# Kernel tuning notes

Measured on AMD Instinct MI355X. Metric: run time of the kernel, lower is better.

Reference implementation:

```python
import jax, jax.numpy as jnp
import numpy as np

TEMPERATURE = 0.03


def setup_inputs() -> dict:
    key = jax.random.key(0)
    k1, k2, k3 = jax.random.split(key, 3)
    B, d = 8192, 256
    z_a = jax.random.normal(k1, (B, d), dtype=jnp.float32)
    z_t = jax.random.normal(k2, (B, d), dtype=jnp.float32)
    # module expects L2-normalized projections
    z_a = z_a / jnp.linalg.norm(z_a, axis=-1, keepdims=True)
    z_t = z_t / jnp.linalg.norm(z_t, axis=-1, keepdims=True)
    patient_ids = jax.random.randint(k3, (B,), 0, 2048, dtype=jnp.int64)
    return {"z_a": z_a, "z_t": z_t, "patient_ids": patient_ids}


def _direction_loss(sim, cross_mask):
    # sim: (B, B) row i = anchor i vs all candidates; cross_mask: (B, B) valid negatives
    B = sim.shape[0]
    pos = jnp.diagonal(sim)                              # (B,) positive logits
    logit_mask = cross_mask | jnp.eye(B, dtype=bool)     # negatives + the positive
    lse = jax.nn.logsumexp(sim, axis=1, where=logit_mask)  # (B,)
    row_loss = lse - pos                                 # CE with label = positive
    valid = cross_mask.any(axis=1)                       # rows with >=1 cross-patient neg
    cnt = jnp.sum(valid)
    total = jnp.sum(jnp.where(valid, row_loss, 0.0))
    return jnp.where(cnt > 0, total / jnp.maximum(cnt, 1).astype(sim.dtype), 0.0)


def reference(z_a, z_t, patient_ids):
    sim = jnp.matmul(z_a, z_t.T) / TEMPERATURE           # (B, B)
    cross = patient_ids[:, None] != patient_ids[None, :] # cross-patient negative mask
    loss_a2t = _direction_loss(sim, cross)
    loss_t2a = _direction_loss(sim.T, cross.T)
    return (loss_a2t + loss_t2a) / 2.0
```

## Files before the change

### kernel.cpp

```cpp
#include <hip/hip_runtime.h>
#include <math.h>

#define BSZ    8192
#define DDIM   256
#define SCALE  33.33333333333333f
#define C_OFF  34.0f
#define SC_L2E 48.08983470f
#define C2     49.05163139f

typedef float floatx4  __attribute__((ext_vector_type(4)));
typedef float floatx16 __attribute__((ext_vector_type(16)));
typedef int   intx4    __attribute__((ext_vector_type(4)));
typedef int   intx8    __attribute__((ext_vector_type(8)));
typedef long long fp8x8;

__device__ __forceinline__ fp8x8 cvt8_f8(const float* __restrict__ g)
{
    const float4 lo = *(const float4*)g;
    const float4 hi = *(const float4*)(g + 4);
    int a = __builtin_amdgcn_cvt_pk_fp8_f32(lo.x, lo.y, 0, false);
    a     = __builtin_amdgcn_cvt_pk_fp8_f32(lo.z, lo.w, a, true);
    int b = __builtin_amdgcn_cvt_pk_fp8_f32(hi.x, hi.y, 0, false);
    b     = __builtin_amdgcn_cvt_pk_fp8_f32(hi.z, hi.w, b, true);
    int2 r; r.x = a; r.y = b;
    return *(fp8x8*)&r;
}

__global__ __launch_bounds__(256) void prep_kernel(
    const float* __restrict__ za, const float* __restrict__ zt,
    unsigned char* __restrict__ za_f8, unsigned char* __restrict__ zt_perm,
    float* __restrict__ zbase)
{
    const int bid = blockIdx.x, tid = threadIdx.x;
    if (bid < 1024) {
        const int i = (bid * 256 + tid) * 8;
        *(fp8x8*)(za_f8 + i) = cvt8_f8(za + i);
        if (bid < 16) {
            const int z = bid * 1024 + tid * 4;
            *(float4*)&zbase[z] = (float4){0.f, 0.f, 0.f, 0.f};
            if (bid == 0 && tid == 0) {
                zbase[16384] = 0.f;
                ((int*)zbase)[16385] = 0;
                ((int*)zbase)[16386] = 0;
            }
        }
    } else {
        const int S    = (bid - 1024) * 256 + tid;
        const int cbb  = S >> 12;
        const int col  = (S >> 5) & 127;
        const int gph  = (S >> 1) & 15;
        const int off8 = (S & 1) * 8;
        const int k    = ((gph ^ (col & 15)) << 4) + off8;
        const float* src = zt + (size_t)(cbb * 128 + col) * DDIM + k;
        *(fp8x8*)(zt_perm + (size_t)S * 8) = cvt8_f8(src);
    }
}

__global__ __launch_bounds__(256, 2) void sim_fused(
    const unsigned char* __restrict__ za_f8, const unsigned char* __restrict__ zt_perm,
    const int* __restrict__ pid,
    float* __restrict__ s_row, float* __restrict__ s_col,
    float* __restrict__ posv)
{
    __shared__ __align__(16) unsigned char Bs[32768];
    __shared__ int   pidc[128];
    __shared__ float colsum[128];

    const int bid   = blockIdx.x;
    const int cbb   = bid & 63;
    const int bgrp  = bid >> 6;
    const int col0g = cbb * 128;
    const int tid   = threadIdx.x, lane = tid & 63, wid = tid >> 6;
    const int l31   = lane & 31, h = lane >> 5;

    if (tid < 128) { pidc[tid] = pid[col0g + tid]; colsum[tid] = 0.f; }

    {
        const unsigned char* src = zt_perm + (size_t)cbb * 32768 + wid * 8192 + lane * 16;
        unsigned char* dst = Bs + wid * 8192 + lane * 16;
        #pragma unroll
        for (int i = 0; i < 8; i++)
            __builtin_amdgcn_global_load_lds(
                (const __attribute__((address_space(1))) void*)(src + i * 1024),
                (__attribute__((address_space(3))) void*)(dst + i * 1024),
                16, 0, 0);
    }

    const int band0 = bgrp * 8;
    intx8 afc[4];
    {
        const unsigned char* ga =
            za_f8 + (size_t)(band0 * 128 + wid * 32 + l31) * DDIM + h * 32;
        #pragma unroll
        for (int ks = 0; ks < 4; ks++)
            afc[ks] = *(const intx8*)(ga + ks * 64);
    }

    __syncthreads();

    const int t16 = ((((lane >> 4) & 2) ^ (lane & 15)) << 4);
    int dsb[4];
    #pragma unroll
    for (int n = 0; n < 4; n++)
        dsb[n] = n * 8192 + l31 * 256 + t16;

    int pc[4];
    #pragma unroll
    for (int n = 0; n < 4; n++) pc[n] = pidc[n * 32 + l31];

    float colp4[4] = {0.f, 0.f, 0.f, 0.f};
    const int  target = (lane & 3) + 4 * ((lane >> 3) & 3);
    const bool ownl   = (h == ((lane >> 2) & 1));

    #pragma unroll
    for (int i = 0; i < 8; i++) {
        const int band  = band0 + i;
        const int rbase = band * 128 + wid * 32;

        intx8 afn[4];
        if (i < 7) {
            const unsigned char* ga =
                za_f8 + (size_t)(rbase + 128 + l31) * DDIM + h * 32;
            #pragma unroll
            for (int ks = 0; ks < 4; ks++)
                afn[ks] = *(const intx8*)(ga + ks * 64);
        }

        int prw[16];
        #pragma unroll
        for (int reg = 0; reg < 16; reg++)
            prw[reg] = pid[rbase + (reg & 3) + 8 * (reg >> 2) + 4 * h];

        floatx16 acc[4];
        #pragma unroll
        for (int n = 0; n < 4; n++) acc[n] = (floatx16)0.0f;

        #pragma unroll
        for (int ks = 0; ks < 4; ks++) {
            #pragma unroll
            for (int n = 0; n < 4; n++) {
                intx4 lo = *(const intx4*)(Bs + (dsb[n] ^ ((ks * 4 + 0) << 4)));
                intx4 hi = *(const intx4*)(Bs + (dsb[n] ^ ((ks * 4 + 1) << 4)));
                intx8 b;
                b[0] = lo[0]; b[1] = lo[1]; b[2] = lo[2]; b[3] = lo[3];
                b[4] = hi[0]; b[5] = hi[1]; b[6] = hi[2]; b[7] = hi[3];
                acc[n] = __builtin_amdgcn_mfma_scale_f32_32x32x64_f8f6f4(
                    afc[ks], b, acc[n], 0, 0, 0, 0x7F7F7F7F, 0, 0x7F7F7F7F);
            }
        }

        float rowp[16];
        #pragma unroll
        for (int r = 0; r < 16; r++) rowp[r] = 0.f;

        #pragma unroll
        for (int n = 0; n < 4; n++) {
            const int pcn = pc[n];
            #pragma unroll
            for (int reg = 0; reg < 16; reg++) {
                float e = __builtin_amdgcn_exp2f(fmaf(acc[n][reg], SC_L2E, -C2));
                e = (prw[reg] != pcn) ? e : 0.f;
                colp4[n] += e;
                rowp[reg] += e;
            }
            if (band == cbb && n == wid) {
                float vd = 0.f;
                #pragma unroll
                for (int reg = 0; reg < 16; reg++)
                    vd = (reg == target) ? acc[n][reg] : vd;
                float ed = __builtin_amdgcn_exp2f(fmaf(vd, SC_L2E, -C2));
                ed = ownl ? ed : 0.f;
                colp4[n] += ed;
                #pragma unroll
                for (int reg = 0; reg < 16; reg++)
                    rowp[reg] += (reg == target) ? ed : 0.f;
                if (ownl) posv[band * 128 + wid * 32 + l31] = vd * SCALE;
            }
        }

#define RED(bit, c)                                                        \
        _Pragma("unroll")                                                  \
        for (int _i = 0; _i < (c); _i++) {                                 \
            float _s = (lane & (bit)) ? rowp[_i] : rowp[_i + (c)];         \
            float _o = __shfl_xor(_s, (bit), 64);                          \
            rowp[_i] = ((lane & (bit)) ? rowp[_i + (c)] : rowp[_i]) + _o;  \
        }
        RED(1, 8) RED(2, 4) RED(4, 2) RED(8, 1)
#undef RED
        rowp[0] += __shfl_xor(rowp[0], 16, 64);
        if ((lane & 16) == 0) {
            const int reg = ((lane & 1) << 3) | ((lane & 2) << 1)
                          | ((lane & 4) >> 1) | ((lane & 8) >> 3);
            const int rl  = (reg & 3) + 8 * (reg >> 2) + 4 * h;
            atomicAdd(&s_row[rbase + rl], rowp[0]);
        }

        if (i < 7) {
            #pragma unroll
            for (int ks = 0; ks < 4; ks++) afc[ks] = afn[ks];
        }
    }

    #pragma unroll
    for (int n = 0; n < 4; n++)
        colp4[n] += __shfl_xor(colp4[n], 32, 64);
    if (lane < 32) {
        #pragma unroll
        for (int n = 0; n < 4; n++)
            atomicAdd(&colsum[n * 32 + lane], colp4[n]);
    }
    __syncthreads();
    if (tid < 128) atomicAdd(&s_col[col0g + tid], colsum[tid]);
}

__global__ __launch_bounds__(256) void finalize_rows(
    const int* __restrict__ pid,
    const float* __restrict__ s_row, const float* __restrict__ s_col,
    const float* __restrict__ posv,
    float* __restrict__ total, int* __restrict__ flag, int* __restrict__ cnt,
    float* __restrict__ out)
{
    const int i = blockIdx.x * 256 + threadIdx.x;
    const float p = posv[i];
    const float c = (logf(s_row[i]) + C_OFF - p)
                  + (logf(s_col[i]) + C_OFF - p);

    float v = c;
    #pragma unroll
    for (int off = 32; off > 0; off >>= 1) v += __shfl_down(v, off, 64);
    if ((threadIdx.x & 63) == 0) atomicAdd(total, v);

    const unsigned long long m = __ballot(pid[i] != pid[0]);
    if (m != 0ull && (threadIdx.x & 63) == 0) atomicOr(flag, 1);

    __syncthreads();
    __threadfence();
    if (threadIdx.x == 0) {
        const int done = atomicAdd(cnt, 1);
        if (done == (int)gridDim.x - 1) {
            const float t = atomicAdd(total, 0.0f);
            const int   f = atomicOr(flag, 0);
            out[0] = f ? t / (2.0f * (float)BSZ) : 0.0f;
        }
    }
}

extern "C" void kernel_launch(void* const* d_in, const int* in_sizes, int n_in,
                              void* d_out, int out_size, void* d_ws, size_t ws_size,
                              hipStream_t stream)
{
    const float* za  = (const float*)d_in[0];
    const float* zt  = (const float*)d_in[1];
    const int*   pid = (const int*)d_in[2];
    float* out = (float*)d_out;

    unsigned char* za_f8   = (unsigned char*)d_ws;
    unsigned char* zt_perm = za_f8 + (size_t)BSZ * DDIM;
    float*  s_row   = (float*)(zt_perm + (size_t)BSZ * DDIM);
    float*  s_col   = s_row + BSZ;
    float*  total   = s_col + BSZ;
    int*    flag    = (int*)(total + 1);
    int*    cnt     = flag + 1;
    float*  posv    = (float*)(cnt + 1);

    prep_kernel<<<dim3(2048), 256, 0, stream>>>(za, zt, za_f8, zt_perm, s_row);

    sim_fused<<<dim3(512), 256, 0, stream>>>(za_f8, zt_perm, pid,
                                             s_row, s_col, posv);

    finalize_rows<<<dim3(BSZ / 256), 256, 0, stream>>>(
        pid, s_row, s_col, posv, total, flag, cnt, out);
}
```

Measured before the change: 102.0 us.

## Fold finalize into sim kernel via grid-wide atomic counter barrier

Removes the separate finalize_rows launch. Each sim_fused block bumps a global counter when it finishes, and the first 32 blocks spin until all 512 blocks are done, then read the row and column sums and the positives atomically and reduce the loss. B-fragment loading is also rewritten as two direct vector stores. This trades a kernel launch for a spin-wait that relies on all 512 blocks being co-resident (2 per CU) to avoid deadlock.

```diff
diff --git a/kernel.cpp b/kernel.cpp
--- a/kernel.cpp
+++ b/kernel.cpp
@@ -42,6 +42,7 @@
                 zbase[16384] = 0.f;
                 ((int*)zbase)[16385] = 0;
                 ((int*)zbase)[16386] = 0;
+                ((int*)zbase)[16387] = 0;
             }
         }
     } else {
@@ -60,7 +61,10 @@
     const unsigned char* __restrict__ za_f8, const unsigned char* __restrict__ zt_perm,
     const int* __restrict__ pid,
     float* __restrict__ s_row, float* __restrict__ s_col,
-    float* __restrict__ posv)
+    float* __restrict__ posv,
+    float* __restrict__ total, int* __restrict__ flag,
+    int* __restrict__ cnt1, int* __restrict__ cnt2,
+    float* __restrict__ out)
 {
     __shared__ __align__(16) unsigned char Bs[32768];
     __shared__ int   pidc[128];
@@ -139,11 +143,11 @@
         for (int ks = 0; ks < 4; ks++) {
             #pragma unroll
             for (int n = 0; n < 4; n++) {
-                intx4 lo = *(const intx4*)(Bs + (dsb[n] ^ ((ks * 4 + 0) << 4)));
-                intx4 hi = *(const intx4*)(Bs + (dsb[n] ^ ((ks * 4 + 1) << 4)));
                 intx8 b;
-                b[0] = lo[0]; b[1] = lo[1]; b[2] = lo[2]; b[3] = lo[3];
-                b[4] = hi[0]; b[5] = hi[1]; b[6] = hi[2]; b[7] = hi[3];
+                *(intx4*)&b =
+                    *(const intx4*)(Bs + (dsb[n] ^ ((ks * 4 + 0) << 4)));
+                *(((intx4*)&b) + 1) =
+                    *(const intx4*)(Bs + (dsb[n] ^ ((ks * 4 + 1) << 4)));
                 acc[n] = __builtin_amdgcn_mfma_scale_f32_32x32x64_f8f6f4(
                     afc[ks], b, acc[n], 0, 0, 0, 0x7F7F7F7F, 0, 0x7F7F7F7F);
             }
@@ -174,7 +178,8 @@
                 #pragma unroll
                 for (int reg = 0; reg < 16; reg++)
                     rowp[reg] += (reg == target) ? ed : 0.f;
-                if (ownl) posv[band * 128 + wid * 32 + l31] = vd * SCALE;
+                if (ownl)
+                    atomicExch(&posv[band * 128 + wid * 32 + l31], vd * SCALE);
             }
         }
 
@@ -211,36 +216,42 @@
     }
     __syncthreads();
     if (tid < 128) atomicAdd(&s_col[col0g + tid], colsum[tid]);
-}
-
-__global__ __launch_bounds__(256) void finalize_rows(
-    const int* __restrict__ pid,
-    const float* __restrict__ s_row, const float* __restrict__ s_col,
-    const float* __restrict__ posv,
-    float* __restrict__ total, int* __restrict__ flag, int* __restrict__ cnt,
-    float* __restrict__ out)
-{
-    const int i = blockIdx.x * 256 + threadIdx.x;
-    const float p = posv[i];
-    const float c = (logf(s_row[i]) + C_OFF - p)
-                  + (logf(s_col[i]) + C_OFF - p);
-
-    float v = c;
-    #pragma unroll
-    for (int off = 32; off > 0; off >>= 1) v += __shfl_down(v, off, 64);
-    if ((threadIdx.x & 63) == 0) atomicAdd(total, v);
-
-    const unsigned long long m = __ballot(pid[i] != pid[0]);
-    if (m != 0ull && (threadIdx.x & 63) == 0) atomicOr(flag, 1);
 
     __syncthreads();
     __threadfence();
-    if (threadIdx.x == 0) {
-        const int done = atomicAdd(cnt, 1);
-        if (done == (int)gridDim.x - 1) {
-            const float t = atomicAdd(total, 0.0f);
-            const int   f = atomicOr(flag, 0);
-            out[0] = f ? t / (2.0f * (float)BSZ) : 0.0f;
+    if (tid == 0) atomicAdd(cnt1, 1);
+    if (bid >= 32) return;
+
+    if (tid == 0) {
+        while (atomicAdd(cnt1, 0) < 512) { __builtin_amdgcn_s_sleep(8); }
+    }
+    __syncthreads();
+
+    {
+        const int i = bid * 256 + tid;
+        const float sr = atomicAdd(&s_row[i], 0.0f);
+        const float sc = atomicAdd(&s_col[i], 0.0f);
+        const float p  = atomicAdd(&posv[i], 0.0f);
+        const float c  = (logf(sr) + C_OFF - p)
+                       + (logf(sc) + C_OFF - p);
+
+        float v = c;
+        #pragma unroll
+        for (int off = 32; off > 0; off >>= 1) v += __shfl_down(v, off, 64);
+        if ((tid & 63) == 0) atomicAdd(total, v);
+
+        const unsigned long long m = __ballot(pid[i] != pid[0]);
+        if (m != 0ull && (tid & 63) == 0) atomicOr(flag, 1);
+
+        __syncthreads();
+        __threadfence();
+        if (tid == 0) {
+            const int done = atomicAdd(cnt2, 1);
+            if (done == 31) {
+                const float t = atomicAdd(total, 0.0f);
+                const int   f = atomicOr(flag, 0);
+                out[0] = f ? t / (2.0f * (float)BSZ) : 0.0f;
+            }
         }
     }
 }
@@ -260,14 +271,13 @@
     float*  s_col   = s_row + BSZ;
     float*  total   = s_col + BSZ;
     int*    flag    = (int*)(total + 1);
-    int*    cnt     = flag + 1;
-    float*  posv    = (float*)(cnt + 1);
+    int*    cnt1    = flag + 1;
+    int*    cnt2    = cnt1 + 1;
+    float*  posv    = (float*)(cnt2 + 1);
 
     prep_kernel<<<dim3(2048), 256, 0, stream>>>(za, zt, za_f8, zt_perm, s_row);
 
     sim_fused<<<dim3(512), 256, 0, stream>>>(za_f8, zt_perm, pid,
-                                             s_row, s_col, posv);
-
-    finalize_rows<<<dim3(BSZ / 256), 256, 0, stream>>>(
-        pid, s_row, s_col, posv, total, flag, cnt, out);
-}
+                                             s_row, s_col, posv,
+                                             total, flag, cnt1, cnt2, out);
+}
```

After: 131.5 us. 1.29x slower.

## Hold the B tile in registers instead of LDS, dropping A prefetch

Applied to the files above, without the earlier changes.

The z_t fp8 permutation is changed to a per-lane MFMA fragment order, so each lane can load its full 128x256 B tile fragments (16 intx8) straight from global memory into registers. This removes the LDS buffer and the per-iteration LDS reads. The double-buffered A prefetch across bands is also removed, and A is now loaded at the start of each band. The launch-bounds occupancy hint of 2 is dropped. The change adds 128 VGPRs per lane for B, which may lower occupancy, and the now unprefetched A loads may be exposed.

```diff
diff --git a/kernel.cpp b/kernel.cpp
--- a/kernel.cpp
+++ b/kernel.cpp
@@ -47,22 +47,25 @@
     } else {
         const int S    = (bid - 1024) * 256 + tid;
         const int cbb  = S >> 12;
-        const int col  = (S >> 5) & 127;
-        const int gph  = (S >> 1) & 15;
-        const int off8 = (S & 1) * 8;
-        const int k    = ((gph ^ (col & 15)) << 4) + off8;
-        const float* src = zt + (size_t)(cbb * 128 + col) * DDIM + k;
+        const int r    = S & 4095;
+        const int o    = r >> 8;
+        const int w    = r & 255;
+        const int ln   = w >> 2;
+        const int part = w & 3;
+        const int ks   = o >> 2, n = o & 3;
+        const int col  = cbb * 128 + n * 32 + (ln & 31);
+        const int k    = ks * 64 + (ln >> 5) * 32 + part * 8;
+        const float* src = zt + (size_t)col * DDIM + k;
         *(fp8x8*)(zt_perm + (size_t)S * 8) = cvt8_f8(src);
     }
 }
 
-__global__ __launch_bounds__(256, 2) void sim_fused(
+__global__ __launch_bounds__(256) void sim_fused(
     const unsigned char* __restrict__ za_f8, const unsigned char* __restrict__ zt_perm,
     const int* __restrict__ pid,
     float* __restrict__ s_row, float* __restrict__ s_col,
     float* __restrict__ posv)
 {
-    __shared__ __align__(16) unsigned char Bs[32768];
     __shared__ int   pidc[128];
     __shared__ float colsum[128];
 
@@ -75,39 +78,23 @@
 
     if (tid < 128) { pidc[tid] = pid[col0g + tid]; colsum[tid] = 0.f; }
 
+    intx8 bf[4][4];
     {
-        const unsigned char* src = zt_perm + (size_t)cbb * 32768 + wid * 8192 + lane * 16;
-        unsigned char* dst = Bs + wid * 8192 + lane * 16;
-        #pragma unroll
-        for (int i = 0; i < 8; i++)
-            __builtin_amdgcn_global_load_lds(
-                (const __attribute__((address_space(1))) void*)(src + i * 1024),
-                (__attribute__((address_space(3))) void*)(dst + i * 1024),
-                16, 0, 0);
-    }
+        const unsigned char* gb = zt_perm + (size_t)cbb * 32768 + lane * 32;
+        #pragma unroll
+        for (int ks = 0; ks < 4; ks++)
+            #pragma unroll
+            for (int n = 0; n < 4; n++)
+                bf[ks][n] = *(const intx8*)(gb + (ks * 4 + n) * 2048);
+    }
+
+    __syncthreads();
+
+    int pc[4];
+    #pragma unroll
+    for (int n = 0; n < 4; n++) pc[n] = pidc[n * 32 + l31];
 
     const int band0 = bgrp * 8;
-    intx8 afc[4];
-    {
-        const unsigned char* ga =
-            za_f8 + (size_t)(band0 * 128 + wid * 32 + l31) * DDIM + h * 32;
-        #pragma unroll
-        for (int ks = 0; ks < 4; ks++)
-            afc[ks] = *(const intx8*)(ga + ks * 64);
-    }
-
-    __syncthreads();
-
-    const int t16 = ((((lane >> 4) & 2) ^ (lane & 15)) << 4);
-    int dsb[4];
-    #pragma unroll
-    for (int n = 0; n < 4; n++)
-        dsb[n] = n * 8192 + l31 * 256 + t16;
-
-    int pc[4];
-    #pragma unroll
-    for (int n = 0; n < 4; n++) pc[n] = pidc[n * 32 + l31];
-
     float colp4[4] = {0.f, 0.f, 0.f, 0.f};
     const int  target = (lane & 3) + 4 * ((lane >> 3) & 3);
     const bool ownl   = (h == ((lane >> 2) & 1));
@@ -117,13 +104,13 @@
         const int band  = band0 + i;
         const int rbase = band * 128 + wid * 32;
 
-        intx8 afn[4];
-        if (i < 7) {
+        intx8 afc[4];
+        {
             const unsigned char* ga =
-                za_f8 + (size_t)(rbase + 128 + l31) * DDIM + h * 32;
+                za_f8 + (size_t)(rbase + l31) * DDIM + h * 32;
             #pragma unroll
             for (int ks = 0; ks < 4; ks++)
-                afn[ks] = *(const intx8*)(ga + ks * 64);
+                afc[ks] = *(const intx8*)(ga + ks * 64);
         }
 
         int prw[16];
@@ -136,18 +123,12 @@
         for (int n = 0; n < 4; n++) acc[n] = (floatx16)0.0f;
 
         #pragma unroll
-        for (int ks = 0; ks < 4; ks++) {
-            #pragma unroll
-            for (int n = 0; n < 4; n++) {
-                intx4 lo = *(const intx4*)(Bs + (dsb[n] ^ ((ks * 4 + 0) << 4)));
-                intx4 hi = *(const intx4*)(Bs + (dsb[n] ^ ((ks * 4 + 1) << 4)));
-                intx8 b;
-                b[0] = lo[0]; b[1] = lo[1]; b[2] = lo[2]; b[3] = lo[3];
-                b[4] = hi[0]; b[5] = hi[1]; b[6] = hi[2]; b[7] = hi[3];
+        for (int ks = 0; ks < 4; ks++)
+            #pragma unroll
+            for (int n = 0; n < 4; n++)
                 acc[n] = __builtin_amdgcn_mfma_scale_f32_32x32x64_f8f6f4(
-                    afc[ks], b, acc[n], 0, 0, 0, 0x7F7F7F7F, 0, 0x7F7F7F7F);
-            }
-        }
+                    afc[ks], bf[ks][n], acc[n], 0, 0, 0,
+                    0x7F7F7F7F, 0, 0x7F7F7F7F);
 
         float rowp[16];
         #pragma unroll
@@ -194,11 +175,6 @@
             const int rl  = (reg & 3) + 8 * (reg >> 2) + 4 * h;
             atomicAdd(&s_row[rbase + rl], rowp[0]);
         }
-
-        if (i < 7) {
-            #pragma unroll
-            for (int ks = 0; ks < 4; ks++) afc[ks] = afn[ks];
-        }
     }
 
     #pragma unroll
```

After: 115.5 us. +13.3%, slower.
